# Optimization experiments

Measured on AMD Instinct MI355X. Metric: run time of the kernel, lower is better.

The kernel has to match this reference:

```python
import jax, jax.numpy as jnp
import numpy as np

B, N, F, MID, OUT, T = 4, 384, 128, 128, 128, 8


def _lin(key, fi, fo):
    W = jax.random.normal(key, (fi, fo), jnp.float32) / np.float32(np.sqrt(fi))
    b = jnp.zeros((fo,), jnp.float32)
    return W, b


def setup_inputs() -> dict:
    key = jax.random.key(0)
    ks = jax.random.split(key, 24)
    inp = {
        "node_fts": jax.random.normal(ks[0], (B, N, F), jnp.float32),
        "edge_fts": jax.random.normal(ks[1], (B, N, N, F), jnp.float32),
        "graph_fts": jax.random.normal(ks[2], (B, F), jnp.float32),
        "adj_mat": jax.random.randint(ks[3], (B, N, N), 0, 2).astype(jnp.float32),
        "hidden": jax.random.normal(ks[4], (B, N, F), jnp.float32),
    }
    i = 5
    for nm in ["m1", "m2", "me", "mg"]:
        W, b = _lin(ks[i], F, MID); inp["W_" + nm], inp["b_" + nm] = W, b; i += 1
    for nm in ["o1", "o2", "o3"]:
        fi = MID if nm == "o3" else F
        W, b = _lin(ks[i], fi, OUT); inp["W_" + nm], inp["b_" + nm] = W, b; i += 1
    for nm in ["tn1", "tn2", "th1", "th2", "te1", "te2", "tg1", "tg2"]:
        W, b = _lin(ks[i], F, T); inp["W_" + nm], inp["b_" + nm] = W, b; i += 1
    return inp


def reference(node_fts, edge_fts, graph_fts, adj_mat, hidden,
              W_m1, b_m1, W_m2, b_m2, W_me, b_me, W_mg, b_mg,
              W_o1, b_o1, W_o2, b_o2, W_o3, b_o3,
              W_tn1, b_tn1, W_tn2, b_tn2, W_th1, b_th1, W_th2, b_th2,
              W_te1, b_te1, W_te2, b_te2, W_tg1, b_tg1, W_tg2, b_tg2):
    # --- triplet-style messages, shape (b, n, n, T) ---
    tn1 = node_fts @ W_tn1 + b_tn1   # (b,n,T)
    tn2 = node_fts @ W_tn2 + b_tn2
    th1 = hidden @ W_th1 + b_th1
    th2 = hidden @ W_th2 + b_th2
    te1 = edge_fts @ W_te1 + b_te1   # (b,n,n,T)
    te2 = edge_fts @ W_te2 + b_te2
    tg1 = graph_fts @ W_tg1 + b_tg1  # (b,T)
    tg2 = graph_fts @ W_tg2 + b_tg2
    tri_msgs = jax.nn.relu(
        tn1[:, None] + tn2[:, :, None]
        + th1[:, None] + th2[:, :, None]
        + te1 + te2
        + tg1[:, None, None] + tg2[:, None, None])

    # --- main MPNN messages, shape (b, n, n, mid) ---
    msg_n = node_fts @ W_m1 + b_m1   # (b,n,mid)
    msg_h = hidden @ W_m2 + b_m2     # (b,n,mid)
    msg_e = edge_fts @ W_me + b_me   # (b,n,n,mid)
    msg_g = graph_fts @ W_mg + b_mg  # (b,mid)
    msgs = (msg_n[:, None] + msg_h[:, :, None]
            + msg_e + msg_g[:, None, None])          # (b,n,n,mid)
    msgs = jnp.max(msgs * adj_mat[..., None], axis=1)  # masked max over senders -> (b,n,mid)

    ret = (node_fts @ W_o1 + b_o1
           + hidden @ W_o2 + b_o2
           + msgs @ W_o3 + b_o3)
    return (ret, tri_msgs)
```

## Files before the change

kernel.cpp:

```cpp
#include <hip/hip_runtime.h>
#include <cstdint>
#include <cstddef>

#define Bb 4
#define Nn 384
#define Ff 128
#define Tt 8

typedef __attribute__((ext_vector_type(8))) __bf16 bf16x8;
typedef __attribute__((ext_vector_type(4))) float fv4;

static __device__ __forceinline__ unsigned int pack2bf(float lo, float hi) {
    union { float f; unsigned int i; } ca, cb;
    ca.f = lo; cb.f = hi;
    unsigned int a = (ca.i + 0x7fffu + ((ca.i >> 16) & 1u)) >> 16;
    unsigned int b = (cb.i + 0x7fffu + ((cb.i >> 16) & 1u)) & 0xffff0000u;
    return a | b;
}
static __device__ __forceinline__ unsigned short f2bf(float f) {
    union { float f; unsigned int i; } c; c.f = f;
    return (unsigned short)((c.i + 0x7fffu + ((c.i >> 16) & 1u)) >> 16);
}
static __device__ __forceinline__ float bf2f(unsigned short u) {
    union { unsigned int i; float f; } c; c.i = ((unsigned int)u) << 16;
    return c.f;
}

__global__ __launch_bounds__(128) void k_pre(
    const float* __restrict__ node, const float* __restrict__ hidden,
    const float* __restrict__ graph,
    const float* __restrict__ W_m1, const float* __restrict__ b_m1,
    const float* __restrict__ W_m2, const float* __restrict__ b_m2,
    const float* __restrict__ b_me,
    const float* __restrict__ W_mg, const float* __restrict__ b_mg,
    const float* __restrict__ W_tn1, const float* __restrict__ b_tn1,
    const float* __restrict__ W_tn2, const float* __restrict__ b_tn2,
    const float* __restrict__ W_th1, const float* __restrict__ b_th1,
    const float* __restrict__ W_th2, const float* __restrict__ b_th2,
    const float* __restrict__ W_tg1, const float* __restrict__ b_tg1,
    const float* __restrict__ W_tg2, const float* __restrict__ b_tg2,
    const float* __restrict__ b_te1, const float* __restrict__ b_te2,
    float* __restrict__ preA, float* __restrict__ preB,
    float* __restrict__ triA, float* __restrict__ triB)
{
    int bn = blockIdx.x;
    int b  = bn / Nn;
    int t  = threadIdx.x;
    __shared__ float sn[Ff], sh[Ff], sg[Ff];
    sn[t] = node[(size_t)bn * Ff + t];
    sh[t] = hidden[(size_t)bn * Ff + t];
    sg[t] = graph[b * Ff + t];
    __syncthreads();

    float a = b_m1[t] + b_mg[t] + b_me[t];
    float h = b_m2[t];
    for (int k = 0; k < Ff; ++k) {
        a = fmaf(sn[k], W_m1[k * Ff + t], a);
        a = fmaf(sg[k], W_mg[k * Ff + t], a);
        h = fmaf(sh[k], W_m2[k * Ff + t], h);
    }
    preA[(size_t)bn * Ff + t] = a;
    preB[(size_t)bn * Ff + t] = h;

    if (t < 2 * Tt) {
        int tt = t & 7;
        if (t < Tt) {
            float v = b_tn1[tt] + b_th1[tt] + b_tg1[tt] + b_tg2[tt] + b_te1[tt] + b_te2[tt];
            for (int k = 0; k < Ff; ++k)
                v += sn[k] * W_tn1[k * Tt + tt] + sh[k] * W_th1[k * Tt + tt]
                   + sg[k] * (W_tg1[k * Tt + tt] + W_tg2[k * Tt + tt]);
            triA[bn * Tt + tt] = v;
        } else {
            float v = b_tn2[tt] + b_th2[tt];
            for (int k = 0; k < Ff; ++k)
                v += sn[k] * W_tn2[k * Tt + tt] + sh[k] * W_th2[k * Tt + tt];
            triB[bn * Tt + tt] = v;
        }
    }
}

__global__ __launch_bounds__(256) void k_prew(
    const float* __restrict__ W_me, const float* __restrict__ W_te1,
    const float* __restrict__ W_te2, unsigned short* __restrict__ wt)
{
    int idx = blockIdx.x * 256 + threadIdx.x;
    if (idx >= 144 * 136) return;
    int row = idx / 136, kc = idx % 136;
    float v = 0.f;
    if (kc < 128) {
        if (row < 128)      v = W_me[kc * Ff + row];
        else if (row < 136) v = W_te1[kc * Tt + (row - 128)] + W_te2[kc * Tt + (row - 128)];
    }
    wt[idx] = f2bf(v);
}

#define EST 136
#define LDS_E_BYTES (64 * EST * 2)
#define LDS_WT_OFF  LDS_E_BYTES
#define LDS_WT_BYTES (144 * EST * 2)
#define LDS_ADJ_OFF (LDS_WT_OFF + LDS_WT_BYTES)
#define LDS_TOTAL   (LDS_ADJ_OFF + 512 * 2)

__global__ __launch_bounds__(256, 2) void k_main(
    const float* __restrict__ edge, const float* __restrict__ adj,
    const unsigned short* __restrict__ wt,
    const float* __restrict__ preB,
    const float* __restrict__ triA, const float* __restrict__ triB,
    unsigned short* __restrict__ partial,
    float* __restrict__ azp,
    float* __restrict__ tri_out)
{
    __shared__ char smem[LDS_TOTAL];
    unsigned short* E   = (unsigned short*)smem;
    unsigned short* WT  = (unsigned short*)(smem + LDS_WT_OFF);
    unsigned short* ADJ = (unsigned short*)(smem + LDS_ADJ_OFF);

    int bx   = blockIdx.x;
    int iblk = bx % 24, jblk = (bx / 24) % 12, b = bx / 288;
    int i0 = iblk * 16, j0 = jblk * 32;
    int t    = threadIdx.x;
    int lane = t & 63, w = t >> 6;
    int l15  = lane & 15, quad = lane >> 4;
    int ih = w >> 1, jh = w & 1;
    int rowbase = ih * 32 + jh * 16;

    for (int idx = t; idx < LDS_WT_BYTES / 16; idx += 256)
        ((uint4*)WT)[idx] = ((const uint4*)wt)[idx];
    for (int idx = t; idx < 512; idx += 256) {
        int il = idx >> 5, jl = idx & 31;
        ADJ[idx] = f2bf(adj[(size_t)(b * Nn + i0 + il) * Nn + j0 + jl]);
    }

    float mx[8][4];
    #pragma unroll
    for (int nt = 0; nt < 8; ++nt)
        #pragma unroll
        for (int r = 0; r < 4; ++r) mx[nt][r] = -1e30f;

    for (int c = 0; c < 8; ++c) {
        __syncthreads();
        const size_t base = ((size_t)(b * Nn + i0 + c * 2) * Nn + j0) * Ff;
        #pragma unroll
        for (int s = 0; s < 8; ++s) {
            int u = t + s * 256;
            int k4 = u & 31, row = u >> 5;
            int il2 = row >> 5, jl2 = row & 31;
            float4 v = *(const float4*)&edge[base + (size_t)il2 * Nn * Ff + (size_t)jl2 * Ff + k4 * 4];
            *(uint2*)&E[row * EST + k4 * 4] = make_uint2(pack2bf(v.x, v.y), pack2bf(v.z, v.w));
        }
        __syncthreads();

        fv4 acc[8]; fv4 at;
        #pragma unroll
        for (int nt = 0; nt < 8; ++nt) acc[nt] = (fv4){0.f, 0.f, 0.f, 0.f};
        at = (fv4){0.f, 0.f, 0.f, 0.f};

        #pragma unroll
        for (int kk = 0; kk < 4; ++kk) {
            int ko = kk * 32 + quad * 8;
            bf16x8 a  = *(const bf16x8*)&E[(rowbase + l15) * EST + ko];
            bf16x8 bt = *(const bf16x8*)&WT[(128 + l15) * EST + ko];
            at = __builtin_amdgcn_mfma_f32_16x16x32_bf16(a, bt, at, 0, 0, 0);
            #pragma unroll
            for (int nt = 0; nt < 8; ++nt) {
                bf16x8 bq = *(const bf16x8*)&WT[(nt * 16 + l15) * EST + ko];
                acc[nt] = __builtin_amdgcn_mfma_f32_16x16x32_bf16(a, bq, acc[nt], 0, 0, 0);
            }
        }

        int il  = c * 2 + ih;
        int i_g = i0 + il;
        const float* pbp = &preB[(size_t)(b * Nn + i_g) * Ff];
        float pbv[8];
        #pragma unroll
        for (int nt = 0; nt < 8; ++nt) pbv[nt] = pbp[nt * 16 + l15];
        float tbv = triB[(b * Nn + i_g) * Tt + (l15 & 7)];
        #pragma unroll
        for (int r = 0; r < 4; ++r) {
            int jl = jh * 16 + quad * 4 + r;
            float adjv = bf2f(ADJ[il * 32 + jl]);
            float mr = fmaf(adjv, 1e30f, -1e30f);
            #pragma unroll
            for (int nt = 0; nt < 8; ++nt)
                mx[nt][r] = fmaxf(mx[nt][r], acc[nt][r] + pbv[nt] + mr);
            float tv = at[r] + triA[(b * Nn + j0 + jl) * Tt + (l15 & 7)] + tbv;
            if (l15 < 8)
                tri_out[((size_t)(b * Nn + i_g) * Nn + j0 + jl) * Tt + l15] = fmaxf(tv, 0.f);
        }
    }

    __syncthreads();
    float* S = (float*)smem;
    #pragma unroll
    for (int r = 0; r < 4; ++r) {
        int jq = quad * 4 + r;
        #pragma unroll
        for (int nt = 0; nt < 8; ++nt)
            S[w * 2048 + jq * 128 + nt * 16 + l15] = mx[nt][r];
    }
    if (t < 32) {
        int any0 = 0;
        for (int il2 = 0; il2 < 16; ++il2) any0 |= (ADJ[il2 * 32 + t] == 0);
        azp[iblk * 1536 + b * Nn + j0 + t] = any0 ? 1.f : 0.f;
    }
    __syncthreads();
    #pragma unroll
    for (int e = 0; e < 16; ++e) {
        int idx = e * 256 + t;
        int jl = idx >> 7, m = idx & 127;
        int jh2 = jl >> 4, jq = jl & 15;
        float v = fmaxf(S[jh2 * 2048 + jq * 128 + m], S[(jh2 + 2) * 2048 + jq * 128 + m]);
        partial[(size_t)iblk * 196608 + (size_t)(b * Nn + j0 + jl) * Ff + m] = f2bf(v);
    }
}

__global__ __launch_bounds__(256) void k_red(
    const unsigned short* __restrict__ partial, const float* __restrict__ azp,
    const float* __restrict__ preA, float* __restrict__ msgs)
{
    int flat = blockIdx.x * 256 + threadIdx.x;
    float v = -1e30f;
    #pragma unroll
    for (int ib = 0; ib < 24; ++ib)
        v = fmaxf(v, bf2f(partial[(size_t)ib * 196608 + flat]));
    float az = 0.f;
    int bj = flat >> 7;
    #pragma unroll
    for (int ib = 0; ib < 24; ++ib) az += azp[ib * 1536 + bj];
    v += preA[flat];
    if (az > 0.5f) v = fmaxf(v, 0.f);
    msgs[flat] = v;
}

__global__ __launch_bounds__(128) void k_out(
    const float* __restrict__ node, const float* __restrict__ hidden,
    const float* __restrict__ msgs_max,
    const float* __restrict__ W_o1, const float* __restrict__ b_o1,
    const float* __restrict__ W_o2, const float* __restrict__ b_o2,
    const float* __restrict__ W_o3, const float* __restrict__ b_o3,
    float* __restrict__ out)
{
    int bn = blockIdx.x;
    int t  = threadIdx.x;
    __shared__ float sn[Ff], sh[Ff], sm[Ff];
    sn[t] = node[(size_t)bn * Ff + t];
    sh[t] = hidden[(size_t)bn * Ff + t];
    sm[t] = msgs_max[(size_t)bn * Ff + t];
    __syncthreads();
    float v = b_o1[t] + b_o2[t] + b_o3[t];
    for (int k = 0; k < Ff; ++k) {
        v = fmaf(sn[k], W_o1[k * Ff + t], v);
        v = fmaf(sh[k], W_o2[k * Ff + t], v);
        v = fmaf(sm[k], W_o3[k * Ff + t], v);
    }
    out[(size_t)bn * Ff + t] = v;
}

extern "C" void kernel_launch(void* const* d_in, const int* in_sizes, int n_in,
                              void* d_out, int out_size, void* d_ws, size_t ws_size,
                              hipStream_t stream)
{
    const float* node   = (const float*)d_in[0];
    const float* edge   = (const float*)d_in[1];
    const float* graph  = (const float*)d_in[2];
    const float* adj    = (const float*)d_in[3];
    const float* hidden = (const float*)d_in[4];
    const float* W_m1 = (const float*)d_in[5];  const float* b_m1 = (const float*)d_in[6];
    const float* W_m2 = (const float*)d_in[7];  const float* b_m2 = (const float*)d_in[8];
    const float* W_me = (const float*)d_in[9];  const float* b_me = (const float*)d_in[10];
    const float* W_mg = (const float*)d_in[11]; const float* b_mg = (const float*)d_in[12];
    const float* W_o1 = (const float*)d_in[13]; const float* b_o1 = (const float*)d_in[14];
    const float* W_o2 = (const float*)d_in[15]; const float* b_o2 = (const float*)d_in[16];
    const float* W_o3 = (const float*)d_in[17]; const float* b_o3 = (const float*)d_in[18];
    const float* W_tn1 = (const float*)d_in[19]; const float* b_tn1 = (const float*)d_in[20];
    const float* W_tn2 = (const float*)d_in[21]; const float* b_tn2 = (const float*)d_in[22];
    const float* W_th1 = (const float*)d_in[23]; const float* b_th1 = (const float*)d_in[24];
    const float* W_th2 = (const float*)d_in[25]; const float* b_th2 = (const float*)d_in[26];
    const float* W_te1 = (const float*)d_in[27]; const float* b_te1 = (const float*)d_in[28];
    const float* W_te2 = (const float*)d_in[29]; const float* b_te2 = (const float*)d_in[30];
    const float* W_tg1 = (const float*)d_in[31]; const float* b_tg1 = (const float*)d_in[32];
    const float* W_tg2 = (const float*)d_in[33]; const float* b_tg2 = (const float*)d_in[34];

    float* ws   = (float*)d_ws;
    float* preA = ws;
    float* preB = preA + 196608;
    float* triA = preB + 196608;
    float* triB = triA + 12288;
    float* msgs = triB + 12288;
    unsigned short* wt      = (unsigned short*)(msgs + 196608);
    unsigned short* partial = wt + 19584;
    float* azp              = (float*)(partial + 4718592);

    float* ret = (float*)d_out;
    float* tri = ret + (size_t)Bb * Nn * Ff;

    hipLaunchKernelGGL(k_pre, dim3(Bb * Nn), dim3(128), 0, stream,
        node, hidden, graph, W_m1, b_m1, W_m2, b_m2, b_me, W_mg, b_mg,
        W_tn1, b_tn1, W_tn2, b_tn2, W_th1, b_th1, W_th2, b_th2,
        W_tg1, b_tg1, W_tg2, b_tg2, b_te1, b_te2,
        preA, preB, triA, triB);
    hipLaunchKernelGGL(k_prew, dim3(77), dim3(256), 0, stream,
        W_me, W_te1, W_te2, wt);
    hipLaunchKernelGGL(k_main, dim3(Bb * 12 * 24), dim3(256), 0, stream,
        edge, adj, wt, preB, triA, triB, partial, azp, tri);
    hipLaunchKernelGGL(k_red, dim3(768), dim3(256), 0, stream,
        partial, azp, preA, msgs);
    hipLaunchKernelGGL(k_out, dim3(Bb * Nn), dim3(128), 0, stream,
        node, hidden, msgs, W_o1, b_o1, W_o2, b_o2, W_o3, b_o3, ret);
}
```

Baseline: 614.6 us.

## Load edge tiles into registers with prefetch and reduce max via atomics

The main kernel stops staging edge tiles through LDS. Each wave loads its A fragments straight from global memory into registers and prefetches the next row pair while converting the current one. Block tiles grow to 24 sender rows, occupancy is raised to 3 blocks, and triA and adj are cached in LDS. The bf16 partial buffer and the separate reduction kernel are replaced by float-ordered integer atomicMax into a buffer initialised in k_pre, with atomicOr for the zero-adjacency flag. This removes a kernel launch and a large partial write and read, at the cost of atomic contention and register pressure.

```diff
diff --git a/kernel.cpp b/kernel.cpp
--- a/kernel.cpp
+++ b/kernel.cpp
@@ -20,10 +20,6 @@
 static __device__ __forceinline__ unsigned short f2bf(float f) {
     union { float f; unsigned int i; } c; c.f = f;
     return (unsigned short)((c.i + 0x7fffu + ((c.i >> 16) & 1u)) >> 16);
-}
-static __device__ __forceinline__ float bf2f(unsigned short u) {
-    union { unsigned int i; float f; } c; c.i = ((unsigned int)u) << 16;
-    return c.f;
 }
 
 __global__ __launch_bounds__(128) void k_pre(
@@ -41,7 +37,8 @@
     const float* __restrict__ W_tg2, const float* __restrict__ b_tg2,
     const float* __restrict__ b_te1, const float* __restrict__ b_te2,
     float* __restrict__ preA, float* __restrict__ preB,
-    float* __restrict__ triA, float* __restrict__ triB)
+    float* __restrict__ triA, float* __restrict__ triB,
+    int* __restrict__ msgs_i, int* __restrict__ az)
 {
     int bn = blockIdx.x;
     int b  = bn / Nn;
@@ -61,6 +58,8 @@
     }
     preA[(size_t)bn * Ff + t] = a;
     preB[(size_t)bn * Ff + t] = h;
+    msgs_i[(size_t)bn * Ff + t] = (int)0x80000000;
+    if (t == 0) az[bn] = 0;
 
     if (t < 2 * Tt) {
         int tt = t & 7;
@@ -95,41 +94,38 @@
 }
 
 #define EST 136
-#define LDS_E_BYTES (64 * EST * 2)
-#define LDS_WT_OFF  LDS_E_BYTES
-#define LDS_WT_BYTES (144 * EST * 2)
-#define LDS_ADJ_OFF (LDS_WT_OFF + LDS_WT_BYTES)
-#define LDS_TOTAL   (LDS_ADJ_OFF + 512 * 2)
-
-__global__ __launch_bounds__(256, 2) void k_main(
+#define WT_ROWS 144
+#define LDS_WT  (WT_ROWS * EST * 2)
+#define LDS_TA  (32 * 8 * 4)
+#define LDS_ADJ (24 * 32 * 4)
+
+__global__ __launch_bounds__(256, 3) void k_main(
     const float* __restrict__ edge, const float* __restrict__ adj,
     const unsigned short* __restrict__ wt,
     const float* __restrict__ preB,
     const float* __restrict__ triA, const float* __restrict__ triB,
-    unsigned short* __restrict__ partial,
-    float* __restrict__ azp,
+    int* __restrict__ msgs_i, int* __restrict__ az,
     float* __restrict__ tri_out)
 {
-    __shared__ char smem[LDS_TOTAL];
-    unsigned short* E   = (unsigned short*)smem;
-    unsigned short* WT  = (unsigned short*)(smem + LDS_WT_OFF);
-    unsigned short* ADJ = (unsigned short*)(smem + LDS_ADJ_OFF);
+    __shared__ char smem[LDS_WT + LDS_TA + LDS_ADJ];
+    unsigned short* WT  = (unsigned short*)smem;
+    float*          sTA = (float*)(smem + LDS_WT);
+    float*          sADJ= (float*)(smem + LDS_WT + LDS_TA);
 
     int bx   = blockIdx.x;
-    int iblk = bx % 24, jblk = (bx / 24) % 12, b = bx / 288;
-    int i0 = iblk * 16, j0 = jblk * 32;
-    int t    = threadIdx.x;
-    int lane = t & 63, w = t >> 6;
-    int l15  = lane & 15, quad = lane >> 4;
+    int iblk = bx & 15, jblk = (bx >> 4) % 12, b = bx / 192;
+    int i0 = iblk * 24, j0 = jblk * 32;
+    int t = threadIdx.x, lane = t & 63, w = t >> 6;
+    int l15 = lane & 15, quad = lane >> 4;
     int ih = w >> 1, jh = w & 1;
-    int rowbase = ih * 32 + jh * 16;
-
-    for (int idx = t; idx < LDS_WT_BYTES / 16; idx += 256)
+
+    for (int idx = t; idx < LDS_WT / 16; idx += 256)
         ((uint4*)WT)[idx] = ((const uint4*)wt)[idx];
-    for (int idx = t; idx < 512; idx += 256) {
-        int il = idx >> 5, jl = idx & 31;
-        ADJ[idx] = f2bf(adj[(size_t)(b * Nn + i0 + il) * Nn + j0 + jl]);
-    }
+    if (t < 256)
+        sTA[t] = triA[(b * Nn + j0 + (t >> 3)) * Tt + (t & 7)];
+    for (int idx = t; idx < 768; idx += 256)
+        sADJ[idx] = adj[(size_t)(b * Nn + i0 + (idx >> 5)) * Nn + j0 + (idx & 31)];
+    __syncthreads();
 
     float mx[8][4];
     #pragma unroll
@@ -137,20 +133,39 @@
         #pragma unroll
         for (int r = 0; r < 4; ++r) mx[nt][r] = -1e30f;
 
-    for (int c = 0; c < 8; ++c) {
-        __syncthreads();
-        const size_t base = ((size_t)(b * Nn + i0 + c * 2) * Nn + j0) * Ff;
-        #pragma unroll
-        for (int s = 0; s < 8; ++s) {
-            int u = t + s * 256;
-            int k4 = u & 31, row = u >> 5;
-            int il2 = row >> 5, jl2 = row & 31;
-            float4 v = *(const float4*)&edge[base + (size_t)il2 * Nn * Ff + (size_t)jl2 * Ff + k4 * 4];
-            *(uint2*)&E[row * EST + k4 * 4] = make_uint2(pack2bf(v.x, v.y), pack2bf(v.z, v.w));
-        }
-        __syncthreads();
-
-        fv4 acc[8]; fv4 at;
+    const float* ebase = edge + ((size_t)(b * Nn + i0 + ih) * Nn + j0 + jh * 16 + l15) * Ff + quad * 8;
+
+    float4 c0[4], c1[4];
+    #pragma unroll
+    for (int kk = 0; kk < 4; ++kk) {
+        c0[kk] = *(const float4*)(ebase + kk * 32);
+        c1[kk] = *(const float4*)(ebase + kk * 32 + 4);
+    }
+
+    for (int c = 0; c < 12; ++c) {
+        int il  = c * 2 + ih;
+        int i_g = i0 + il;
+
+        bf16x8 af[4];
+        #pragma unroll
+        for (int kk = 0; kk < 4; ++kk) {
+            union { uint4 u; bf16x8 v; } cv;
+            cv.u.x = pack2bf(c0[kk].x, c0[kk].y);
+            cv.u.y = pack2bf(c0[kk].z, c0[kk].w);
+            cv.u.z = pack2bf(c1[kk].x, c1[kk].y);
+            cv.u.w = pack2bf(c1[kk].z, c1[kk].w);
+            af[kk] = cv.v;
+        }
+        if (c + 1 < 12) {
+            const float* p = ebase + (size_t)(c + 1) * (2 * Nn * Ff);
+            #pragma unroll
+            for (int kk = 0; kk < 4; ++kk) {
+                c0[kk] = *(const float4*)(p + kk * 32);
+                c1[kk] = *(const float4*)(p + kk * 32 + 4);
+            }
+        }
+
+        fv4 acc[8], at;
         #pragma unroll
         for (int nt = 0; nt < 8; ++nt) acc[nt] = (fv4){0.f, 0.f, 0.f, 0.f};
         at = (fv4){0.f, 0.f, 0.f, 0.f};
@@ -158,18 +173,15 @@
         #pragma unroll
         for (int kk = 0; kk < 4; ++kk) {
             int ko = kk * 32 + quad * 8;
-            bf16x8 a  = *(const bf16x8*)&E[(rowbase + l15) * EST + ko];
             bf16x8 bt = *(const bf16x8*)&WT[(128 + l15) * EST + ko];
-            at = __builtin_amdgcn_mfma_f32_16x16x32_bf16(a, bt, at, 0, 0, 0);
+            at = __builtin_amdgcn_mfma_f32_16x16x32_bf16(af[kk], bt, at, 0, 0, 0);
             #pragma unroll
             for (int nt = 0; nt < 8; ++nt) {
                 bf16x8 bq = *(const bf16x8*)&WT[(nt * 16 + l15) * EST + ko];
-                acc[nt] = __builtin_amdgcn_mfma_f32_16x16x32_bf16(a, bq, acc[nt], 0, 0, 0);
+                acc[nt] = __builtin_amdgcn_mfma_f32_16x16x32_bf16(af[kk], bq, acc[nt], 0, 0, 0);
             }
         }
 
-        int il  = c * 2 + ih;
-        int i_g = i0 + il;
         const float* pbp = &preB[(size_t)(b * Nn + i_g) * Ff];
         float pbv[8];
         #pragma unroll
@@ -178,12 +190,12 @@
         #pragma unroll
         for (int r = 0; r < 4; ++r) {
             int jl = jh * 16 + quad * 4 + r;
-            float adjv = bf2f(ADJ[il * 32 + jl]);
+            float adjv = sADJ[il * 32 + jl];
             float mr = fmaf(adjv, 1e30f, -1e30f);
             #pragma unroll
             for (int nt = 0; nt < 8; ++nt)
                 mx[nt][r] = fmaxf(mx[nt][r], acc[nt][r] + pbv[nt] + mr);
-            float tv = at[r] + triA[(b * Nn + j0 + jl) * Tt + (l15 & 7)] + tbv;
+            float tv = at[r] + sTA[jl * 8 + (l15 & 7)] + tbv;
             if (l15 < 8)
                 tri_out[((size_t)(b * Nn + i_g) * Nn + j0 + jl) * Tt + l15] = fmaxf(tv, 0.f);
         }
@@ -200,8 +212,8 @@
     }
     if (t < 32) {
         int any0 = 0;
-        for (int il2 = 0; il2 < 16; ++il2) any0 |= (ADJ[il2 * 32 + t] == 0);
-        azp[iblk * 1536 + b * Nn + j0 + t] = any0 ? 1.f : 0.f;
+        for (int il2 = 0; il2 < 24; ++il2) any0 |= (sADJ[il2 * 32 + t] == 0.f);
+        if (any0) atomicOr(&az[b * Nn + j0 + t], 1);
     }
     __syncthreads();
     #pragma unroll
@@ -210,31 +222,16 @@
         int jl = idx >> 7, m = idx & 127;
         int jh2 = jl >> 4, jq = jl & 15;
         float v = fmaxf(S[jh2 * 2048 + jq * 128 + m], S[(jh2 + 2) * 2048 + jq * 128 + m]);
-        partial[(size_t)iblk * 196608 + (size_t)(b * Nn + j0 + jl) * Ff + m] = f2bf(v);
-    }
-}
-
-__global__ __launch_bounds__(256) void k_red(
-    const unsigned short* __restrict__ partial, const float* __restrict__ azp,
-    const float* __restrict__ preA, float* __restrict__ msgs)
-{
-    int flat = blockIdx.x * 256 + threadIdx.x;
-    float v = -1e30f;
-    #pragma unroll
-    for (int ib = 0; ib < 24; ++ib)
-        v = fmaxf(v, bf2f(partial[(size_t)ib * 196608 + flat]));
-    float az = 0.f;
-    int bj = flat >> 7;
-    #pragma unroll
-    for (int ib = 0; ib < 24; ++ib) az += azp[ib * 1536 + bj];
-    v += preA[flat];
-    if (az > 0.5f) v = fmaxf(v, 0.f);
-    msgs[flat] = v;
+        int iv  = __float_as_int(v);
+        int key = iv >= 0 ? iv : (iv ^ 0x7fffffff);
+        atomicMax(&msgs_i[(size_t)(b * Nn + j0 + jl) * Ff + m], key);
+    }
 }
 
 __global__ __launch_bounds__(128) void k_out(
     const float* __restrict__ node, const float* __restrict__ hidden,
-    const float* __restrict__ msgs_max,
+    const int* __restrict__ msgs_i, const int* __restrict__ az,
+    const float* __restrict__ preA,
     const float* __restrict__ W_o1, const float* __restrict__ b_o1,
     const float* __restrict__ W_o2, const float* __restrict__ b_o2,
     const float* __restrict__ W_o3, const float* __restrict__ b_o3,
@@ -245,7 +242,11 @@
     __shared__ float sn[Ff], sh[Ff], sm[Ff];
     sn[t] = node[(size_t)bn * Ff + t];
     sh[t] = hidden[(size_t)bn * Ff + t];
-    sm[t] = msgs_max[(size_t)bn * Ff + t];
+    int iv = msgs_i[(size_t)bn * Ff + t];
+    int dk = iv >= 0 ? iv : (iv ^ 0x7fffffff);
+    float mv = __int_as_float(dk) + preA[(size_t)bn * Ff + t];
+    if (az[bn] != 0) mv = fmaxf(mv, 0.f);
+    sm[t] = mv;
     __syncthreads();
     float v = b_o1[t] + b_o2[t] + b_o3[t];
     for (int k = 0; k < Ff; ++k) {
@@ -286,10 +287,9 @@
     float* preB = preA + 196608;
     float* triA = preB + 196608;
     float* triB = triA + 12288;
-    float* msgs = triB + 12288;
-    unsigned short* wt      = (unsigned short*)(msgs + 196608);
-    unsigned short* partial = wt + 19584;
-    float* azp              = (float*)(partial + 4718592);
+    int*   msgs_i = (int*)(triB + 12288);
+    int*   az     = msgs_i + 196608;
+    unsigned short* wt = (unsigned short*)(az + 1536);
 
     float* ret = (float*)d_out;
     float* tri = ret + (size_t)Bb * Nn * Ff;
@@ -298,13 +298,11 @@
         node, hidden, graph, W_m1, b_m1, W_m2, b_m2, b_me, W_mg, b_mg,
         W_tn1, b_tn1, W_tn2, b_tn2, W_th1, b_th1, W_th2, b_th2,
         W_tg1, b_tg1, W_tg2, b_tg2, b_te1, b_te2,
-        preA, preB, triA, triB);
+        preA, preB, triA, triB, msgs_i, az);
     hipLaunchKernelGGL(k_prew, dim3(77), dim3(256), 0, stream,
         W_me, W_te1, W_te2, wt);
-    hipLaunchKernelGGL(k_main, dim3(Bb * 12 * 24), dim3(256), 0, stream,
-        edge, adj, wt, preB, triA, triB, partial, azp, tri);
-    hipLaunchKernelGGL(k_red, dim3(768), dim3(256), 0, stream,
-        partial, azp, preA, msgs);
+    hipLaunchKernelGGL(k_main, dim3(768), dim3(256), 0, stream,
+        edge, adj, wt, preB, triA, triB, msgs_i, az, tri);
     hipLaunchKernelGGL(k_out, dim3(Bb * Nn), dim3(128), 0, stream,
-        node, hidden, msgs, W_o1, b_o1, W_o2, b_o2, W_o3, b_o3, ret);
-}
+        node, hidden, msgs_i, az, preA, W_o1, b_o1, W_o2, b_o2, W_o3, b_o3, ret);
+}
```

Result: slower. 719.2 us (+17.0%).
